# Kernel optimization log

Measured on AMD Instinct MI355X. Metric: run time of the kernel, lower is better.

The kernel has to match this reference:

```python
import jax, jax.numpy as jnp
import numpy as np

D_MODEL = 512
D_FF = 2048
NUM_EXPERTS = 8
TOP_K = 2


def setup_inputs() -> dict:
    key = jax.random.key(0)
    ks = jax.random.split(key, 6)
    scale = 0.02
    x = jax.random.normal(ks[0], (4, 8192, D_MODEL), dtype=jnp.float32)
    gate_w = jax.random.normal(ks[1], (D_MODEL, NUM_EXPERTS), dtype=jnp.float32) * scale
    w1 = jax.random.normal(ks[2], (NUM_EXPERTS, D_MODEL, D_FF), dtype=jnp.float32) * scale
    b1 = jnp.zeros((NUM_EXPERTS, D_FF), dtype=jnp.float32)
    w2 = jax.random.normal(ks[3], (NUM_EXPERTS, D_FF, D_MODEL), dtype=jnp.float32) * scale
    b2 = jnp.zeros((NUM_EXPERTS, D_MODEL), dtype=jnp.float32)
    return {"x": x, "gate_w": gate_w, "w1": w1, "b1": b1, "w2": w2, "b2": b2}


def reference(x, gate_w, w1, b1, w2, b2):
    B, S, D = x.shape
    xt = x.reshape(-1, D)                                  # [T, D]
    logits = xt @ gate_w                                   # [T, E]
    probs = jax.nn.softmax(logits, axis=-1)
    top_p, top_i = jax.lax.top_k(probs, TOP_K)             # [T, K]
    top_p = top_p / jnp.sum(top_p, axis=-1, keepdims=True)
    # per-token combine weight for each expert: [T, E]
    w_te = jnp.sum(jax.nn.one_hot(top_i, NUM_EXPERTS, dtype=xt.dtype) * top_p[..., None], axis=1)
    out = jnp.zeros_like(xt)
    for e in range(NUM_EXPERTS):  # small fixed loop over experts
        h = jax.nn.gelu(xt @ w1[e] + b1[e], approximate=False)  # [T, d_ff]
        y = h @ w2[e] + b2[e]                                   # [T, D]
        out = out + w_te[:, e:e + 1] * y
    return out.reshape(B, S, D)
```

## Files before the change

kernel.cpp:

```cpp
#include <hip/hip_runtime.h>
#include <math.h>

#define T_TOK 32768
#define DM 512
#define DFF 2048
#define NE 8
#define MAXTILES 528

typedef __attribute__((ext_vector_type(8))) short short8;
typedef __attribute__((ext_vector_type(4))) float f32x4;

__device__ __forceinline__ unsigned int f2bf1(float f) {
  union { float f; unsigned int u; } x; x.f = f;
  return (x.u + 0x7fffu + ((x.u >> 16) & 1u)) >> 16;
}

__global__ void tcvt_kernel(const float* __restrict__ src, unsigned short* __restrict__ dst,
                            int R, int C) {
  __shared__ float tile[32][33];
  int e = blockIdx.z;
  const float* s = src + (size_t)e * R * C;
  unsigned short* d = dst + (size_t)e * R * C;
  int c0 = blockIdx.x * 32, r0 = blockIdx.y * 32;
  int tx = threadIdx.x, ty = threadIdx.y;
#pragma unroll
  for (int i = 0; i < 4; ++i)
    tile[ty + i * 8][tx] = s[(size_t)(r0 + ty + i * 8) * C + c0 + tx];
  __syncthreads();
#pragma unroll
  for (int i = 0; i < 4; ++i)
    d[(size_t)(c0 + ty + i * 8) * R + r0 + tx] = (unsigned short)f2bf1(tile[tx][ty + i * 8]);
}

__global__ __launch_bounds__(1024) void gate_kernel(
    const float* __restrict__ x, const float* __restrict__ gw,
    int* __restrict__ cnt, int* __restrict__ tok, float* __restrict__ wgt,
    unsigned int* __restrict__ xb) {
  __shared__ int lcnt[NE];
  __shared__ int lbase[NE];
  __shared__ int wslot[16][2];
  __shared__ int winfo[16][2];
  __shared__ float wval[16][2];
  int tid = threadIdx.x;
  int wid = tid >> 6, lane = tid & 63;
  int t = blockIdx.x * 16 + wid;
  if (tid < NE) lcnt[tid] = 0;
  __syncthreads();

  float acc[NE];
#pragma unroll
  for (int e = 0; e < NE; ++e) acc[e] = 0.f;
  const float* xr = x + (size_t)t * DM;
  unsigned int* xbr = xb + (size_t)t * (DM / 2);
#pragma unroll
  for (int j = 0; j < 4; ++j) {
    int d0 = j * 128 + lane * 2;
    float2 xv = *(const float2*)(xr + d0);
    const float* g0 = gw + d0 * NE;
#pragma unroll
    for (int e = 0; e < NE; ++e) acc[e] += xv.x * g0[e] + xv.y * g0[NE + e];
    xbr[j * 64 + lane] = f2bf1(xv.x) | (f2bf1(xv.y) << 16);
  }
#pragma unroll
  for (int off = 32; off >= 1; off >>= 1) {
#pragma unroll
    for (int e = 0; e < NE; ++e) acc[e] += __shfl_xor(acc[e], off);
  }
  if (lane == 0) {
    int e0 = 0; float l0 = acc[0];
#pragma unroll
    for (int e = 1; e < NE; ++e) if (acc[e] > l0) { l0 = acc[e]; e0 = e; }
    int e1 = (e0 == 0) ? 1 : 0; float l1 = acc[e1];
#pragma unroll
    for (int e = 0; e < NE; ++e) if (e != e0 && acc[e] > l1) { l1 = acc[e]; e1 = e; }
    float w0 = 1.f / (1.f + expf(l1 - l0));
    winfo[wid][0] = e0; winfo[wid][1] = e1;
    wval[wid][0] = w0;  wval[wid][1] = 1.f - w0;
    wslot[wid][0] = atomicAdd(&lcnt[e0], 1);
    wslot[wid][1] = atomicAdd(&lcnt[e1], 1);
  }
  __syncthreads();
  if (tid < NE) lbase[tid] = atomicAdd(&cnt[tid * 64], lcnt[tid]);
  __syncthreads();
  if (lane == 0) {
    int e0 = winfo[wid][0], e1 = winfo[wid][1];
    int p0 = lbase[e0] + wslot[wid][0];
    int p1 = lbase[e1] + wslot[wid][1];
    tok[e0 * T_TOK + p0] = t; wgt[e0 * T_TOK + p0] = wval[wid][0];
    tok[e1 * T_TOK + p1] = t; wgt[e1 * T_TOK + p1] = wval[wid][1];
  }
}

__global__ void plan_kernel(const int* __restrict__ cnt, int* __restrict__ tile_base) {
  if (threadIdx.x == 0 && blockIdx.x == 0) {
    int tb = 0;
    for (int e = 0; e < NE; ++e) { tile_base[e] = tb; tb += (cnt[e * 64] + 127) >> 7; }
    tile_base[NE] = tb;
  }
}

__global__ __launch_bounds__(256) void gemm1_kernel(
    const unsigned int* __restrict__ xb, const unsigned short* __restrict__ w1t,
    const float* __restrict__ b1, const int* __restrict__ cnt,
    const int* __restrict__ tok, const int* __restrict__ tile_base,
    unsigned short* __restrict__ H, int tile_lo) {
  int bid = (int)blockIdx.x;
  int nt = bid & 15;
  int gt = tile_lo + (bid >> 4);
  if (gt >= tile_base[NE]) return;
  int e = 0;
#pragma unroll
  for (int k = 0; k < NE - 1; ++k) e += (gt >= tile_base[k + 1]) ? 1 : 0;
  int tloc = gt - tile_base[e];
  int ce = cnt[e * 64];
  int m0 = tloc * 128;
  int n0 = nt * 128;

  __shared__ unsigned short As[128 * 32];
  __shared__ unsigned short Bs[128 * 32];

  int tid = (int)threadIdx.x;
  int lane = tid & 63;
  int wid = tid >> 6;
  int wm = wid & 1, wn = wid >> 1;
  int fl = lane & 15, q = lane >> 4;
  int sxy = ((q ^ ((fl >> 1) & 3)) << 4);

  const int* tokg = tok + e * T_TOK;
  int r0 = tid >> 2, r1 = 64 + (tid >> 2);
  int sl = tid & 3;
  int ss0 = sl ^ ((r0 >> 1) & 3);
  int ss1 = sl ^ ((r1 >> 1) & 3);
  int t0 = tokg[min(m0 + r0, ce - 1)];
  int t1 = tokg[min(m0 + r1, ce - 1)];
  const char* asrc0 = (const char*)xb + (size_t)t0 * 1024 + ss0 * 16;
  const char* asrc1 = (const char*)xb + (size_t)t1 * 1024 + ss1 * 16;
  const char* bsrc0 = (const char*)w1t + ((size_t)e * DFF + n0 + r0) * 1024 + ss0 * 16;
  const char* bsrc1 = (const char*)w1t + ((size_t)e * DFF + n0 + r1) * 1024 + ss1 * 16;
  char* adst0 = (char*)As + tid * 16;
  char* adst1 = (char*)As + 4096 + tid * 16;
  char* bdst0 = (char*)Bs + tid * 16;
  char* bdst1 = (char*)Bs + 4096 + tid * 16;

  int aoff[4], boff[4];
#pragma unroll
  for (int i = 0; i < 4; ++i) {
    aoff[i] = (wm * 64 + i * 16 + fl) * 64 + sxy;
    boff[i] = (wn * 64 + i * 16 + fl) * 64 + sxy;
  }

  f32x4 acc[4][4];
#pragma unroll
  for (int a = 0; a < 4; ++a)
#pragma unroll
    for (int b = 0; b < 4; ++b) acc[a][b] = (f32x4){0.f, 0.f, 0.f, 0.f};

  for (int t = 0; t < 16; ++t) {
    size_t ko = (size_t)t * 64;
    __builtin_amdgcn_global_load_lds((const __attribute__((address_space(1))) unsigned int*)(asrc0 + ko),
                                     (__attribute__((address_space(3))) unsigned int*)adst0, 16, 0, 0);
    __builtin_amdgcn_global_load_lds((const __attribute__((address_space(1))) unsigned int*)(asrc1 + ko),
                                     (__attribute__((address_space(3))) unsigned int*)adst1, 16, 0, 0);
    __builtin_amdgcn_global_load_lds((const __attribute__((address_space(1))) unsigned int*)(bsrc0 + ko),
                                     (__attribute__((address_space(3))) unsigned int*)bdst0, 16, 0, 0);
    __builtin_amdgcn_global_load_lds((const __attribute__((address_space(1))) unsigned int*)(bsrc1 + ko),
                                     (__attribute__((address_space(3))) unsigned int*)bdst1, 16, 0, 0);
    __syncthreads();
    short8 a[4], b[4];
#pragma unroll
    for (int i = 0; i < 4; ++i) {
      a[i] = *(const short8*)((const char*)As + aoff[i]);
      b[i] = *(const short8*)((const char*)Bs + boff[i]);
    }
#pragma unroll
    for (int mf = 0; mf < 4; ++mf)
#pragma unroll
      for (int nf = 0; nf < 4; ++nf)
        acc[mf][nf] = __builtin_amdgcn_mfma_f32_16x16x32_bf16(a[mf], b[nf], acc[mf][nf], 0, 0, 0);
    __syncthreads();
  }

  size_t hrow0 = (size_t)(gt - tile_lo) * 128;
#pragma unroll
  for (int nf = 0; nf < 4; ++nf) {
    float bias = b1[e * DFF + n0 + wn * 64 + nf * 16 + fl];
    int col = n0 + wn * 64 + nf * 16 + fl;
#pragma unroll
    for (int mf = 0; mf < 4; ++mf)
#pragma unroll
      for (int j = 0; j < 4; ++j) {
        int row = wm * 64 + mf * 16 + q * 4 + j;
        float v = acc[mf][nf][j] + bias;
        v = 0.5f * v * (1.f + erff(v * 0.70710678118654752f));
        H[(hrow0 + row) * DFF + col] = (unsigned short)f2bf1(v);
      }
  }
}

__global__ __launch_bounds__(256) void gemm2_kernel(
    const unsigned short* __restrict__ H, const unsigned short* __restrict__ w2t,
    const float* __restrict__ b2, const int* __restrict__ cnt,
    const int* __restrict__ tok, const float* __restrict__ wgt,
    const int* __restrict__ tile_base, float* __restrict__ out, int tile_lo) {
  int bid = (int)blockIdx.x;
  int nt = bid & 3;
  int gt = tile_lo + (bid >> 2);
  if (gt >= tile_base[NE]) return;
  int e = 0;
#pragma unroll
  for (int k = 0; k < NE - 1; ++k) e += (gt >= tile_base[k + 1]) ? 1 : 0;
  int tloc = gt - tile_base[e];
  int ce = cnt[e * 64];
  int m0 = tloc * 128;
  int n0 = nt * 128;

  __shared__ unsigned short As[128 * 32];
  __shared__ unsigned short Bs[128 * 32];

  int tid = (int)threadIdx.x;
  int lane = tid & 63;
  int wid = tid >> 6;
  int wm = wid & 1, wn = wid >> 1;
  int fl = lane & 15, q = lane >> 4;
  int sxy = ((q ^ ((fl >> 1) & 3)) << 4);

  int r0 = tid >> 2, r1 = 64 + (tid >> 2);
  int sl = tid & 3;
  int ss0 = sl ^ ((r0 >> 1) & 3);
  int ss1 = sl ^ ((r1 >> 1) & 3);
  size_t hrow0 = (size_t)(gt - tile_lo) * 128;
  const char* asrc0 = (const char*)H + (hrow0 + r0) * 4096 + ss0 * 16;
  const char* asrc1 = (const char*)H + (hrow0 + r1) * 4096 + ss1 * 16;
  const char* bsrc0 = (const char*)w2t + ((size_t)e * DM + n0 + r0) * 4096 + ss0 * 16;
  const char* bsrc1 = (const char*)w2t + ((size_t)e * DM + n0 + r1) * 4096 + ss1 * 16;
  char* adst0 = (char*)As + tid * 16;
  char* adst1 = (char*)As + 4096 + tid * 16;
  char* bdst0 = (char*)Bs + tid * 16;
  char* bdst1 = (char*)Bs + 4096 + tid * 16;

  int aoff[4], boff[4];
#pragma unroll
  for (int i = 0; i < 4; ++i) {
    aoff[i] = (wm * 64 + i * 16 + fl) * 64 + sxy;
    boff[i] = (wn * 64 + i * 16 + fl) * 64 + sxy;
  }

  f32x4 acc[4][4];
#pragma unroll
  for (int a = 0; a < 4; ++a)
#pragma unroll
    for (int b = 0; b < 4; ++b) acc[a][b] = (f32x4){0.f, 0.f, 0.f, 0.f};

  for (int t = 0; t < 64; ++t) {
    size_t ko = (size_t)t * 64;
    __builtin_amdgcn_global_load_lds((const __attribute__((address_space(1))) unsigned int*)(asrc0 + ko),
                                     (__attribute__((address_space(3))) unsigned int*)adst0, 16, 0, 0);
    __builtin_amdgcn_global_load_lds((const __attribute__((address_space(1))) unsigned int*)(asrc1 + ko),
                                     (__attribute__((address_space(3))) unsigned int*)adst1, 16, 0, 0);
    __builtin_amdgcn_global_load_lds((const __attribute__((address_space(1))) unsigned int*)(bsrc0 + ko),
                                     (__attribute__((address_space(3))) unsigned int*)bdst0, 16, 0, 0);
    __builtin_amdgcn_global_load_lds((const __attribute__((address_space(1))) unsigned int*)(bsrc1 + ko),
                                     (__attribute__((address_space(3))) unsigned int*)bdst1, 16, 0, 0);
    __syncthreads();
    short8 a[4], b[4];
#pragma unroll
    for (int i = 0; i < 4; ++i) {
      a[i] = *(const short8*)((const char*)As + aoff[i]);
      b[i] = *(const short8*)((const char*)Bs + boff[i]);
    }
#pragma unroll
    for (int mf = 0; mf < 4; ++mf)
#pragma unroll
      for (int nf = 0; nf < 4; ++nf)
        acc[mf][nf] = __builtin_amdgcn_mfma_f32_16x16x32_bf16(a[mf], b[nf], acc[mf][nf], 0, 0, 0);
    __syncthreads();
  }

  const int* tokg = tok + e * T_TOK;
  const float* wgtg = wgt + e * T_TOK;
  float bias2[4];
#pragma unroll
  for (int nf = 0; nf < 4; ++nf) bias2[nf] = b2[e * DM + n0 + wn * 64 + nf * 16 + fl];
#pragma unroll
  for (int mf = 0; mf < 4; ++mf)
#pragma unroll
    for (int j = 0; j < 4; ++j) {
      int row = wm * 64 + mf * 16 + q * 4 + j;
      int slot = m0 + row;
      if (slot < ce) {
        int tk = tokg[slot];
        float w = wgtg[slot];
        float* orow = out + (size_t)tk * DM + n0 + wn * 64;
#pragma unroll
        for (int nf = 0; nf < 4; ++nf)
          atomicAdd(orow + nf * 16 + fl, w * (acc[mf][nf][j] + bias2[nf]));
      }
    }
}

extern "C" void kernel_launch(void* const* d_in, const int* in_sizes, int n_in,
                              void* d_out, int out_size, void* d_ws, size_t ws_size,
                              hipStream_t stream) {
  (void)in_sizes; (void)n_in; (void)out_size;
  const float* x  = (const float*)d_in[0];
  const float* gw = (const float*)d_in[1];
  const float* w1 = (const float*)d_in[2];
  const float* b1 = (const float*)d_in[3];
  const float* w2 = (const float*)d_in[4];
  const float* b2 = (const float*)d_in[5];
  float* out = (float*)d_out;

  char* ws = (char*)d_ws;
  size_t off = 0;
  auto alloc = [&](size_t sz) { char* p = ws + off; off += (sz + 255) & ~(size_t)255; return p; };
  int*   cnt = (int*)alloc(NE * 64 * 4);
  int*   tok = (int*)alloc((size_t)NE * T_TOK * 4);
  float* wgt = (float*)alloc((size_t)NE * T_TOK * 4);
  int*   tile_base = (int*)alloc((NE + 1) * 4);
  unsigned int* xb = (unsigned int*)alloc((size_t)T_TOK * (DM / 2) * 4);
  unsigned short* w1t = (unsigned short*)alloc((size_t)NE * DFF * DM * 2);
  unsigned short* w2t = (unsigned short*)alloc((size_t)NE * DM * DFF * 2);

  size_t avail = (ws_size > off) ? (ws_size - off) : 0;
  int TPC = MAXTILES, NC = 1;
  while (NC < 32 && (size_t)TPC * 128 * DFF * 2 > avail) {
    NC *= 2; TPC = (MAXTILES + NC - 1) / NC;
  }
  unsigned short* H = (unsigned short*)alloc((size_t)TPC * 128 * DFF * 2);

  hipMemsetAsync(cnt, 0, NE * 64 * 4, stream);
  hipMemsetAsync(out, 0, (size_t)T_TOK * DM * 4, stream);

  tcvt_kernel<<<dim3(DFF / 32, DM / 32, NE), dim3(32, 8), 0, stream>>>(w1, w1t, DM, DFF);
  tcvt_kernel<<<dim3(DM / 32, DFF / 32, NE), dim3(32, 8), 0, stream>>>(w2, w2t, DFF, DM);
  gate_kernel<<<T_TOK / 16, 1024, 0, stream>>>(x, gw, cnt, tok, wgt, xb);
  plan_kernel<<<1, 64, 0, stream>>>(cnt, tile_base);

  for (int c = 0; c < NC; ++c) {
    int lo = c * TPC;
    if (lo >= MAXTILES) break;
    gemm1_kernel<<<TPC * 16, 256, 0, stream>>>(xb, w1t, b1, cnt, tok, tile_base, H, lo);
    gemm2_kernel<<<TPC * 4, 256, 0, stream>>>(H, w2t, b2, cnt, tok, wgt, tile_base, out, lo);
  }
}
```

Baseline: 664.9 us.

## Double-buffer LDS tiles in both expert GEMM kernels to overlap loads with MFMA

Both grouped GEMM kernels now use two LDS buffers per operand. The next K-slice is issued with global_load_lds while MFMAs run on the current buffer, and the loop is unrolled by two, with one barrier per slice instead of two. The aim is to hide global-to-LDS latency behind matrix compute. LDS per block doubles to 32 KB, which may reduce occupancy. Correctness relies on the compiler's waitcnt placement before each barrier.

```diff
diff --git a/kernel.cpp b/kernel.cpp
--- a/kernel.cpp
+++ b/kernel.cpp
@@ -14,6 +14,10 @@
   union { float f; unsigned int u; } x; x.f = f;
   return (x.u + 0x7fffu + ((x.u >> 16) & 1u)) >> 16;
 }
+
+#define GLOAD(src, dst) \
+  __builtin_amdgcn_global_load_lds((const __attribute__((address_space(1))) unsigned int*)(src), \
+                                   (__attribute__((address_space(3))) unsigned int*)(dst), 16, 0, 0)
 
 __global__ void tcvt_kernel(const float* __restrict__ src, unsigned short* __restrict__ dst,
                             int R, int C) {
@@ -116,8 +120,8 @@
   int m0 = tloc * 128;
   int n0 = nt * 128;
 
-  __shared__ unsigned short As[128 * 32];
-  __shared__ unsigned short Bs[128 * 32];
+  __shared__ unsigned short As[2][128 * 32];
+  __shared__ unsigned short Bs[2][128 * 32];
 
   int tid = (int)threadIdx.x;
   int lane = tid & 63;
@@ -137,10 +141,6 @@
   const char* asrc1 = (const char*)xb + (size_t)t1 * 1024 + ss1 * 16;
   const char* bsrc0 = (const char*)w1t + ((size_t)e * DFF + n0 + r0) * 1024 + ss0 * 16;
   const char* bsrc1 = (const char*)w1t + ((size_t)e * DFF + n0 + r1) * 1024 + ss1 * 16;
-  char* adst0 = (char*)As + tid * 16;
-  char* adst1 = (char*)As + 4096 + tid * 16;
-  char* bdst0 = (char*)Bs + tid * 16;
-  char* bdst1 = (char*)Bs + 4096 + tid * 16;
 
   int aoff[4], boff[4];
 #pragma unroll
@@ -155,30 +155,34 @@
 #pragma unroll
     for (int b = 0; b < 4; ++b) acc[a][b] = (f32x4){0.f, 0.f, 0.f, 0.f};
 
-  for (int t = 0; t < 16; ++t) {
-    size_t ko = (size_t)t * 64;
-    __builtin_amdgcn_global_load_lds((const __attribute__((address_space(1))) unsigned int*)(asrc0 + ko),
-                                     (__attribute__((address_space(3))) unsigned int*)adst0, 16, 0, 0);
-    __builtin_amdgcn_global_load_lds((const __attribute__((address_space(1))) unsigned int*)(asrc1 + ko),
-                                     (__attribute__((address_space(3))) unsigned int*)adst1, 16, 0, 0);
-    __builtin_amdgcn_global_load_lds((const __attribute__((address_space(1))) unsigned int*)(bsrc0 + ko),
-                                     (__attribute__((address_space(3))) unsigned int*)bdst0, 16, 0, 0);
-    __builtin_amdgcn_global_load_lds((const __attribute__((address_space(1))) unsigned int*)(bsrc1 + ko),
-                                     (__attribute__((address_space(3))) unsigned int*)bdst1, 16, 0, 0);
+#define STAGE1(AB, BB, ko) do { \
+    GLOAD(asrc0 + (ko), (char*)(AB) + tid * 16);        \
+    GLOAD(asrc1 + (ko), (char*)(AB) + 4096 + tid * 16); \
+    GLOAD(bsrc0 + (ko), (char*)(BB) + tid * 16);        \
+    GLOAD(bsrc1 + (ko), (char*)(BB) + 4096 + tid * 16); } while (0)
+
+#define COMP1(AB, BB) do { \
+    short8 a[4], b[4]; \
+    _Pragma("unroll") for (int i = 0; i < 4; ++i) { \
+      a[i] = *(const short8*)((const char*)(AB) + aoff[i]); \
+      b[i] = *(const short8*)((const char*)(BB) + boff[i]); } \
+    _Pragma("unroll") for (int mf = 0; mf < 4; ++mf) \
+    _Pragma("unroll") for (int nf = 0; nf < 4; ++nf) \
+      acc[mf][nf] = __builtin_amdgcn_mfma_f32_16x16x32_bf16(a[mf], b[nf], acc[mf][nf], 0, 0, 0); \
+  } while (0)
+
+  STAGE1(As[0], Bs[0], 0);
+  __syncthreads();
+  for (int t = 0; t < 16; t += 2) {
+    STAGE1(As[1], Bs[1], (size_t)(t + 1) * 64);
+    COMP1(As[0], Bs[0]);
     __syncthreads();
-    short8 a[4], b[4];
-#pragma unroll
-    for (int i = 0; i < 4; ++i) {
-      a[i] = *(const short8*)((const char*)As + aoff[i]);
-      b[i] = *(const short8*)((const char*)Bs + boff[i]);
-    }
-#pragma unroll
-    for (int mf = 0; mf < 4; ++mf)
-#pragma unroll
-      for (int nf = 0; nf < 4; ++nf)
-        acc[mf][nf] = __builtin_amdgcn_mfma_f32_16x16x32_bf16(a[mf], b[nf], acc[mf][nf], 0, 0, 0);
+    if (t + 2 < 16) STAGE1(As[0], Bs[0], (size_t)(t + 2) * 64);
+    COMP1(As[1], Bs[1]);
     __syncthreads();
   }
+#undef STAGE1
+#undef COMP1
 
   size_t hrow0 = (size_t)(gt - tile_lo) * 128;
 #pragma unroll
@@ -214,8 +218,8 @@
   int m0 = tloc * 128;
   int n0 = nt * 128;
 
-  __shared__ unsigned short As[128 * 32];
-  __shared__ unsigned short Bs[128 * 32];
+  __shared__ unsigned short As[2][128 * 32];
+  __shared__ unsigned short Bs[2][128 * 32];
 
   int tid = (int)threadIdx.x;
   int lane = tid & 63;
@@ -233,10 +237,6 @@
   const char* asrc1 = (const char*)H + (hrow0 + r1) * 4096 + ss1 * 16;
   const char* bsrc0 = (const char*)w2t + ((size_t)e * DM + n0 + r0) * 4096 + ss0 * 16;
   const char* bsrc1 = (const char*)w2t + ((size_t)e * DM + n0 + r1) * 4096 + ss1 * 16;
-  char* adst0 = (char*)As + tid * 16;
-  char* adst1 = (char*)As + 4096 + tid * 16;
-  char* bdst0 = (char*)Bs + tid * 16;
-  char* bdst1 = (char*)Bs + 4096 + tid * 16;
 
   int aoff[4], boff[4];
 #pragma unroll
@@ -251,30 +251,34 @@
 #pragma unroll
     for (int b = 0; b < 4; ++b) acc[a][b] = (f32x4){0.f, 0.f, 0.f, 0.f};
 
-  for (int t = 0; t < 64; ++t) {
-    size_t ko = (size_t)t * 64;
-    __builtin_amdgcn_global_load_lds((const __attribute__((address_space(1))) unsigned int*)(asrc0 + ko),
-                                     (__attribute__((address_space(3))) unsigned int*)adst0, 16, 0, 0);
-    __builtin_amdgcn_global_load_lds((const __attribute__((address_space(1))) unsigned int*)(asrc1 + ko),
-                                     (__attribute__((address_space(3))) unsigned int*)adst1, 16, 0, 0);
-    __builtin_amdgcn_global_load_lds((const __attribute__((address_space(1))) unsigned int*)(bsrc0 + ko),
-                                     (__attribute__((address_space(3))) unsigned int*)bdst0, 16, 0, 0);
-    __builtin_amdgcn_global_load_lds((const __attribute__((address_space(1))) unsigned int*)(bsrc1 + ko),
-                                     (__attribute__((address_space(3))) unsigned int*)bdst1, 16, 0, 0);
+#define STAGE2(AB, BB, ko) do { \
+    GLOAD(asrc0 + (ko), (char*)(AB) + tid * 16);        \
+    GLOAD(asrc1 + (ko), (char*)(AB) + 4096 + tid * 16); \
+    GLOAD(bsrc0 + (ko), (char*)(BB) + tid * 16);        \
+    GLOAD(bsrc1 + (ko), (char*)(BB) + 4096 + tid * 16); } while (0)
+
+#define COMP2(AB, BB) do { \
+    short8 a[4], b[4]; \
+    _Pragma("unroll") for (int i = 0; i < 4; ++i) { \
+      a[i] = *(const short8*)((const char*)(AB) + aoff[i]); \
+      b[i] = *(const short8*)((const char*)(BB) + boff[i]); } \
+    _Pragma("unroll") for (int mf = 0; mf < 4; ++mf) \
+    _Pragma("unroll") for (int nf = 0; nf < 4; ++nf) \
+      acc[mf][nf] = __builtin_amdgcn_mfma_f32_16x16x32_bf16(a[mf], b[nf], acc[mf][nf], 0, 0, 0); \
+  } while (0)
+
+  STAGE2(As[0], Bs[0], 0);
+  __syncthreads();
+  for (int t = 0; t < 64; t += 2) {
+    STAGE2(As[1], Bs[1], (size_t)(t + 1) * 64);
+    COMP2(As[0], Bs[0]);
     __syncthreads();
-    short8 a[4], b[4];
-#pragma unroll
-    for (int i = 0; i < 4; ++i) {
-      a[i] = *(const short8*)((const char*)As + aoff[i]);
-      b[i] = *(const short8*)((const char*)Bs + boff[i]);
-    }
-#pragma unroll
-    for (int mf = 0; mf < 4; ++mf)
-#pragma unroll
-      for (int nf = 0; nf < 4; ++nf)
-        acc[mf][nf] = __builtin_amdgcn_mfma_f32_16x16x32_bf16(a[mf], b[nf], acc[mf][nf], 0, 0, 0);
+    if (t + 2 < 64) STAGE2(As[0], Bs[0], (size_t)(t + 2) * 64);
+    COMP2(As[1], Bs[1]);
     __syncthreads();
   }
+#undef STAGE2
+#undef COMP2
 
   const int* tokg = tok + e * T_TOK;
   const float* wgtg = wgt + e * T_TOK;
```

Measured after the change: 685.9 us. +3.2%, slower.
